# Kernel tuning notes

Measured on AMD Instinct MI355X. Metric: run time of the kernel, lower is better.

Reference implementation:

```python
import jax, jax.numpy as jnp
import numpy as np

N, E, NFEAT, NHID = 8192, 262144, 512, 256


def setup_inputs() -> dict:
    key = jax.random.key(0)
    k_x, k_w, k_b, k_a = jax.random.split(key, 4)
    x = jax.random.normal(k_x, (N, NFEAT), dtype=jnp.float32)
    # unique edges so adj.nonzero()-style edge list has no duplicates
    rng = np.random.default_rng(0)
    flat = rng.choice(N * N, size=E, replace=False)
    edge_index = jnp.asarray(np.stack([flat // N, flat % N]), dtype=jnp.int64)
    adj = jnp.zeros((N, N), dtype=jnp.float32).at[edge_index[0], edge_index[1]].set(1.0)
    W_lin = jax.random.normal(k_w, (NHID, NFEAT), dtype=jnp.float32) / np.sqrt(NFEAT)
    b_lin = jax.random.normal(k_b, (NHID,), dtype=jnp.float32) * 0.01
    W_att = jax.random.normal(k_a, (2 * NHID,), dtype=jnp.float32) / np.sqrt(2 * NHID)
    return {"adj": adj, "x": x, "edge_index": edge_index,
            "W_lin": W_lin, "b_lin": b_lin, "W_att": W_att}


def reference(adj, x, edge_index, W_lin, b_lin, W_att):
    # dropout in eval mode -> identity
    h = x @ W_lin.T + b_lin                      # [N, nhid]
    src, dst = edge_index[0], edge_index[1]
    nhid = h.shape[1]
    # att(concat(h[src], h[dst])) == (h @ a_src)[src] + (h @ a_dst)[dst]
    s = h @ W_att[:nhid]                         # [N]
    t = h @ W_att[nhid:]                         # [N]
    e = jnp.tanh(s[src] + t[dst])                # [E]
    new_adj = jnp.zeros_like(adj).at[src, dst].set(e)  # unique edges: set == sparse to_dense
    return new_adj * adj, h
```

## Files before the change

kernel.cpp:

```cpp
#include <hip/hip_runtime.h>
#include <hip/hip_bf16.h>
#include <cmath>

#define N_NODES 8192
#define E_EDGES 262144
#define NFEAT   512
#define NHID    256

typedef __attribute__((ext_vector_type(8))) short short8;
typedef __attribute__((ext_vector_type(4))) float f32x4;
typedef __attribute__((ext_vector_type(4))) short short4v;

static __device__ inline unsigned short f2bf(float f) {
    union { float f; unsigned u; } v; v.f = f;
    unsigned r = v.u + 0x7FFFu + ((v.u >> 16) & 1u);
    return (unsigned short)(r >> 16);
}

__global__ __launch_bounds__(256) void convw_kernel(
        const float* __restrict__ W, unsigned short* __restrict__ Wbf) {
    const int i = (blockIdx.x * 256 + threadIdx.x) * 4;
    const float4 w = *reinterpret_cast<const float4*>(&W[i]);
    short4v o;
    o[0] = (short)f2bf(w.x); o[1] = (short)f2bf(w.y);
    o[2] = (short)f2bf(w.z); o[3] = (short)f2bf(w.w);
    *reinterpret_cast<short4v*>(&Wbf[i]) = o;
}

__global__ __launch_bounds__(256) void gemm_fused_kernel(
        const float* __restrict__ x,
        const unsigned short* __restrict__ Wbf,
        const float* __restrict__ b,
        const float* __restrict__ Wa,
        float* __restrict__ hout,
        float* __restrict__ s, float* __restrict__ t) {
    const int lane = threadIdx.x & 63;
    const int wave = threadIdx.x >> 6;
    const int r    = lane & 15;
    const int kg   = lane >> 4;
    const int m0   = blockIdx.x * 64 + wave * 16;

    f32x4 acc[16];
    #pragma unroll
    for (int nt = 0; nt < 16; ++nt) acc[nt] = (f32x4)0.0f;

    const float* xrow = x + (size_t)(m0 + r) * NFEAT + kg * 8;

    for (int ks = 0; ks < NFEAT / 32; ++ks) {
        const int k0 = ks * 32;
        short8 af;
        {
            const float4 a0 = *reinterpret_cast<const float4*>(xrow + k0);
            const float4 a1 = *reinterpret_cast<const float4*>(xrow + k0 + 4);
            af[0] = (short)f2bf(a0.x); af[1] = (short)f2bf(a0.y);
            af[2] = (short)f2bf(a0.z); af[3] = (short)f2bf(a0.w);
            af[4] = (short)f2bf(a1.x); af[5] = (short)f2bf(a1.y);
            af[6] = (short)f2bf(a1.z); af[7] = (short)f2bf(a1.w);
        }
        #pragma unroll
        for (int nt = 0; nt < 16; ++nt) {
            const short8 bf = *reinterpret_cast<const short8*>(
                &Wbf[(size_t)(nt * 16 + r) * NFEAT + k0 + kg * 8]);
            acc[nt] = __builtin_amdgcn_mfma_f32_16x16x32_bf16(af, bf, acc[nt], 0, 0, 0);
        }
    }

    float sp[4] = {0.f, 0.f, 0.f, 0.f};
    float tp[4] = {0.f, 0.f, 0.f, 0.f};
    #pragma unroll
    for (int nt = 0; nt < 16; ++nt) {
        const int n   = nt * 16 + r;
        const float bb  = b[n];
        const float was = Wa[n];
        const float wat = Wa[NHID + n];
        #pragma unroll
        for (int j = 0; j < 4; ++j) {
            const float hv = acc[nt][j] + bb;
            hout[(size_t)(m0 + kg * 4 + j) * NHID + n] = hv;
            sp[j] = fmaf(hv, was, sp[j]);
            tp[j] = fmaf(hv, wat, tp[j]);
        }
    }
    #pragma unroll
    for (int off = 1; off < 16; off <<= 1) {
        #pragma unroll
        for (int j = 0; j < 4; ++j) {
            sp[j] += __shfl_xor(sp[j], off);
            tp[j] += __shfl_xor(tp[j], off);
        }
    }
    if (r == 0) {
        #pragma unroll
        for (int j = 0; j < 4; ++j) {
            const int m = m0 + kg * 4 + j;
            s[m] = sp[j];
            t[m] = tp[j];
        }
    }
}

__global__ __launch_bounds__(256) void edge_kernel(
        const int* __restrict__ ei,
        const float* __restrict__ s, const float* __restrict__ t,
        float* __restrict__ out) {
    const int e = blockIdx.x * blockDim.x + threadIdx.x;
    if (e >= E_EDGES) return;
    const int src = ei[e];
    const int dst = ei[E_EDGES + e];
    out[(size_t)src * N_NODES + dst] = tanhf(s[src] + t[dst]);
}

extern "C" void kernel_launch(void* const* d_in, const int* in_sizes, int n_in,
                              void* d_out, int out_size, void* d_ws, size_t ws_size,
                              hipStream_t stream) {
    const float* x    = (const float*)d_in[1];
    const int*   ei   = (const int*)  d_in[2];
    const float* Wlin = (const float*)d_in[3];
    const float* blin = (const float*)d_in[4];
    const float* Watt = (const float*)d_in[5];

    float* out0 = (float*)d_out;
    float* hout = out0 + (size_t)N_NODES * N_NODES;

    unsigned short* Wbf = (unsigned short*)d_ws;
    float* s = (float*)((char*)d_ws + NHID * NFEAT * sizeof(unsigned short));
    float* t = s + N_NODES;

    hipMemsetAsync(out0, 0, (size_t)N_NODES * N_NODES * sizeof(float), stream);

    convw_kernel<<<(NHID * NFEAT / 4) / 256, 256, 0, stream>>>(Wlin, Wbf);

    gemm_fused_kernel<<<N_NODES / 64, 256, 0, stream>>>(
        x, Wbf, blin, Watt, hout, s, t);

    edge_kernel<<<E_EDGES / 256, 256, 0, stream>>>(ei, s, t, out0);
}
```

Baseline: 478.6 us.

## Build CSR of edges and fuse zero-fill with row-wise edge writes; split GEMM N across waves

Replaces the full-matrix memset plus scattered edge writes with a CSR build (count, scan, scatter) and a per-row kernel that zeroes each output row and then writes its edges while the row is likely still cached. The GEMM now gives each block 16 rows with the four waves splitting the hidden columns, which launches four times as many blocks, and the s/t partial sums are combined through shared memory. This adds several small launches, including a single-block scan and atomic-heavy count and scatter passes. The output-write traffic stays about the same.

Result: faster. 465.9 us (-2.6%).

```diff
diff --git a/kernel.cpp b/kernel.cpp
--- a/kernel.cpp
+++ b/kernel.cpp
@@ -38,14 +38,17 @@
     const int wave = threadIdx.x >> 6;
     const int r    = lane & 15;
     const int kg   = lane >> 4;
-    const int m0   = blockIdx.x * 64 + wave * 16;
-
-    f32x4 acc[16];
-    #pragma unroll
-    for (int nt = 0; nt < 16; ++nt) acc[nt] = (f32x4)0.0f;
+    const int m0   = blockIdx.x * 16;
+
+    __shared__ float sred[4][16], tred[4][16];
+
+    f32x4 acc[4];
+    #pragma unroll
+    for (int q = 0; q < 4; ++q) acc[q] = (f32x4)0.0f;
 
     const float* xrow = x + (size_t)(m0 + r) * NFEAT + kg * 8;
 
+    #pragma unroll 4
     for (int ks = 0; ks < NFEAT / 32; ++ks) {
         const int k0 = ks * 32;
         short8 af;
@@ -58,24 +61,25 @@
             af[6] = (short)f2bf(a1.z); af[7] = (short)f2bf(a1.w);
         }
         #pragma unroll
-        for (int nt = 0; nt < 16; ++nt) {
+        for (int q = 0; q < 4; ++q) {
+            const int nt = wave * 4 + q;
             const short8 bf = *reinterpret_cast<const short8*>(
                 &Wbf[(size_t)(nt * 16 + r) * NFEAT + k0 + kg * 8]);
-            acc[nt] = __builtin_amdgcn_mfma_f32_16x16x32_bf16(af, bf, acc[nt], 0, 0, 0);
+            acc[q] = __builtin_amdgcn_mfma_f32_16x16x32_bf16(af, bf, acc[q], 0, 0, 0);
         }
     }
 
     float sp[4] = {0.f, 0.f, 0.f, 0.f};
     float tp[4] = {0.f, 0.f, 0.f, 0.f};
     #pragma unroll
-    for (int nt = 0; nt < 16; ++nt) {
-        const int n   = nt * 16 + r;
+    for (int q = 0; q < 4; ++q) {
+        const int n = (wave * 4 + q) * 16 + r;
         const float bb  = b[n];
         const float was = Wa[n];
         const float wat = Wa[NHID + n];
         #pragma unroll
         for (int j = 0; j < 4; ++j) {
-            const float hv = acc[nt][j] + bb;
+            const float hv = acc[q][j] + bb;
             hout[(size_t)(m0 + kg * 4 + j) * NHID + n] = hv;
             sp[j] = fmaf(hv, was, sp[j]);
             tp[j] = fmaf(hv, wat, tp[j]);
@@ -92,22 +96,81 @@
     if (r == 0) {
         #pragma unroll
         for (int j = 0; j < 4; ++j) {
-            const int m = m0 + kg * 4 + j;
-            s[m] = sp[j];
-            t[m] = tp[j];
-        }
-    }
-}
-
-__global__ __launch_bounds__(256) void edge_kernel(
-        const int* __restrict__ ei,
+            sred[wave][kg * 4 + j] = sp[j];
+            tred[wave][kg * 4 + j] = tp[j];
+        }
+    }
+    __syncthreads();
+    if (threadIdx.x < 16) {
+        const int row = threadIdx.x;
+        float ss = sred[0][row] + sred[1][row] + sred[2][row] + sred[3][row];
+        float tt = tred[0][row] + tred[1][row] + tred[2][row] + tred[3][row];
+        s[m0 + row] = ss;
+        t[m0 + row] = tt;
+    }
+}
+
+__global__ __launch_bounds__(256) void count_kernel(
+        const int* __restrict__ ei, int* __restrict__ counts) {
+    const int e = blockIdx.x * 256 + threadIdx.x;
+    atomicAdd(&counts[ei[e]], 1);
+}
+
+__global__ __launch_bounds__(256) void scan_kernel(
+        const int* __restrict__ counts, int* __restrict__ offsets,
+        int* __restrict__ cursor) {
+    __shared__ int ssum[256];
+    const int t = threadIdx.x;
+    int local[32];
+    int run = 0;
+    #pragma unroll
+    for (int i = 0; i < 32; ++i) { local[i] = run; run += counts[t * 32 + i]; }
+    ssum[t] = run;
+    __syncthreads();
+    for (int off = 1; off < 256; off <<= 1) {
+        int v = ssum[t];
+        if (t >= off) v += ssum[t - off];
+        __syncthreads();
+        ssum[t] = v;
+        __syncthreads();
+    }
+    const int base = (t == 0) ? 0 : ssum[t - 1];
+    #pragma unroll
+    for (int i = 0; i < 32; ++i) {
+        const int o = base + local[i];
+        offsets[t * 32 + i] = o;
+        cursor [t * 32 + i] = o;
+    }
+    if (t == 255) offsets[N_NODES] = ssum[255];
+}
+
+__global__ __launch_bounds__(256) void scatter_kernel(
+        const int* __restrict__ ei, int* __restrict__ cursor,
+        int* __restrict__ col) {
+    const int e = blockIdx.x * 256 + threadIdx.x;
+    const int src = ei[e];
+    const int dst = ei[E_EDGES + e];
+    const int pos = atomicAdd(&cursor[src], 1);
+    col[pos] = dst;
+}
+
+__global__ __launch_bounds__(256) void dense_kernel(
+        const int* __restrict__ offsets, const int* __restrict__ col,
         const float* __restrict__ s, const float* __restrict__ t,
         float* __restrict__ out) {
-    const int e = blockIdx.x * blockDim.x + threadIdx.x;
-    if (e >= E_EDGES) return;
-    const int src = ei[e];
-    const int dst = ei[E_EDGES + e];
-    out[(size_t)src * N_NODES + dst] = tanhf(s[src] + t[dst]);
+    const int row = blockIdx.x;
+    float* orow = out + (size_t)row * N_NODES;
+    const f32x4 z = (f32x4)0.0f;
+    #pragma unroll
+    for (int j = 0; j < 8; ++j)
+        *reinterpret_cast<f32x4*>(orow + (threadIdx.x + j * 256) * 4) = z;
+    __syncthreads();
+    const int beg = offsets[row], end = offsets[row + 1];
+    const float sr = s[row];
+    for (int k = beg + (int)threadIdx.x; k < end; k += 256) {
+        const int dst = col[k];
+        orow[dst] = tanhf(sr + t[dst]);
+    }
 }
 
 extern "C" void kernel_launch(void* const* d_in, const int* in_sizes, int n_in,
@@ -122,16 +185,23 @@
     float* out0 = (float*)d_out;
     float* hout = out0 + (size_t)N_NODES * N_NODES;
 
-    unsigned short* Wbf = (unsigned short*)d_ws;
-    float* s = (float*)((char*)d_ws + NHID * NFEAT * sizeof(unsigned short));
-    float* t = s + N_NODES;
-
-    hipMemsetAsync(out0, 0, (size_t)N_NODES * N_NODES * sizeof(float), stream);
+    char* w = (char*)d_ws;
+    unsigned short* Wbf = (unsigned short*)w;  w += NHID * NFEAT * sizeof(unsigned short);
+    float* s       = (float*)w;                w += N_NODES * sizeof(float);
+    float* t       = (float*)w;                w += N_NODES * sizeof(float);
+    int*   counts  = (int*)w;                  w += N_NODES * sizeof(int);
+    int*   offsets = (int*)w;                  w += (N_NODES + 1) * sizeof(int);
+    int*   cursor  = (int*)w;                  w += N_NODES * sizeof(int);
+    int*   col     = (int*)w;
+
+    hipMemsetAsync(counts, 0, N_NODES * sizeof(int), stream);
+    count_kernel  <<<E_EDGES / 256, 256, 0, stream>>>(ei, counts);
+    scan_kernel   <<<1, 256, 0, stream>>>(counts, offsets, cursor);
+    scatter_kernel<<<E_EDGES / 256, 256, 0, stream>>>(ei, cursor, col);
 
     convw_kernel<<<(NHID * NFEAT / 4) / 256, 256, 0, stream>>>(Wlin, Wbf);
-
-    gemm_fused_kernel<<<N_NODES / 64, 256, 0, stream>>>(
+    gemm_fused_kernel<<<N_NODES / 16, 256, 0, stream>>>(
         x, Wbf, blin, Watt, hout, s, t);
 
-    edge_kernel<<<E_EDGES / 256, 256, 0, stream>>>(ei, s, t, out0);
-}
+    dense_kernel<<<N_NODES, 256, 0, stream>>>(offsets, col, s, t, out0);
+}
```
